# Kernel optimization log

Hardware: AMD Instinct MI355X
Metric: run time of the kernel (lower is better)

## Reference

```python
import jax, jax.numpy as jnp
import numpy as np

DIM = 2048
HEADS = 16
DIM_HEAD = 128
DIM_INNER = HEADS * DIM_HEAD
BATCH = 2
SEQ = 2048
EPS = 1e-12  # F.normalize default eps


def l2norm(t, axis=-1):
    # matches F.normalize(t, dim=axis, p=2): t / max(||t||, eps)
    n = jnp.sqrt(jnp.sum(t * t, axis=axis, keepdims=True))
    return t / jnp.maximum(n, EPS)


def setup_inputs() -> dict:
    key = jax.random.key(0)
    ks = jax.random.split(key, 5)
    x = jax.random.normal(ks[0], (BATCH, SEQ, DIM), dtype=jnp.float32)
    # NormLinear weights (torch Linear layout: [out, in]); parametrization
    # l2-normalizes rows (dim=-1) for q/k/v and columns (dim=0) for to_out.
    Wq = jax.random.normal(ks[1], (DIM_INNER, DIM), dtype=jnp.float32) / np.sqrt(DIM)
    Wk = jax.random.normal(ks[2], (DIM_INNER, DIM), dtype=jnp.float32) / np.sqrt(DIM)
    Wv = jax.random.normal(ks[3], (DIM_INNER, DIM), dtype=jnp.float32) / np.sqrt(DIM)
    Wout = jax.random.normal(ks[4], (DIM, DIM_INNER), dtype=jnp.float32) / np.sqrt(DIM_INNER)
    # Scale(dim_inner, init=1.0, scale=dim**-1): param = ones * dim**-1,
    # forward_scale = init/scale = dim, so qk_scale() starts at 1.0
    qk_scale = jnp.ones((DIM_INNER,), dtype=jnp.float32) / DIM
    return {"x": x, "Wq": Wq, "Wk": Wk, "Wv": Wv, "Wout": Wout, "qk_scale": qk_scale}


def reference(x, Wq, Wk, Wv, Wout, qk_scale):
    b, n, _ = x.shape
    # NormLinear: x @ l2norm(W, rows).T  (scale = groups**-1 = 1)
    q = jnp.einsum('bnd,ed->bne', x, l2norm(Wq, axis=-1))
    k = jnp.einsum('bnd,ed->bne', x, l2norm(Wk, axis=-1))
    v = jnp.einsum('bnd,ed->bne', x, l2norm(Wv, axis=-1))
    # split heads: b n (h d) -> b h n d
    split = lambda t: t.reshape(b, n, HEADS, DIM_HEAD).transpose(0, 2, 1, 3)
    q, k, v = split(q), split(k), split(v)
    # per-head l2norm of q and k over head dim
    q = l2norm(q, axis=-1)
    k = l2norm(k, axis=-1)
    # learned qk scale: (h d) -> h 1 d, effective = param * forward_scale(=DIM)
    q = q * (qk_scale * DIM).reshape(HEADS, 1, DIM_HEAD)
    # causal SDPA with scale = sqrt(dim_head) (unit-norm q,k in nGPT)
    attn_scale = DIM_HEAD ** 0.5
    scores = jnp.einsum('bhid,bhjd->bhij', q, k) * attn_scale
    causal = jnp.tril(jnp.ones((n, n), dtype=bool))
    scores = jnp.where(causal, scores, jnp.finfo(scores.dtype).min)
    attn = jax.nn.softmax(scores, axis=-1)
    out = jnp.einsum('bhij,bhjd->bhid', attn, v)
    # merge heads: b h n d -> b n (h d)
    out = out.transpose(0, 2, 1, 3).reshape(b, n, DIM_INNER)
    # to_out: NormLinear with norm over dim=0 of weight [DIM, DIM_INNER]
    out = jnp.einsum('bne,de->bnd', out, l2norm(Wout, axis=0))
    return out
```

## Files before the change

kernel.cpp:

```cpp
#include <hip/hip_runtime.h>


typedef __bf16 bf16x8 __attribute__((ext_vector_type(8)));
typedef float f32x4 __attribute__((ext_vector_type(4)));

__device__ __forceinline__ unsigned short f2bf(float f) {
  unsigned int u = __float_as_uint(f);
  u = u + 0x7FFFu + ((u >> 16) & 1u);
  return (unsigned short)(u >> 16);
}

__device__ __forceinline__ void async16(const void* g, void* l) {
  __builtin_amdgcn_global_load_lds(
      (const __attribute__((address_space(1))) unsigned int*)g,
      (__attribute__((address_space(3))) unsigned int*)l, 16, 0, 0);
}

#define QFOLD (2048.0f * 11.313708498984761f * 1.4426950408889634f)


__global__ __launch_bounds__(256) void prep_w_rows(
    const float* __restrict__ Wq, const float* __restrict__ Wk,
    const float* __restrict__ Wv, ushort* __restrict__ oq,
    ushort* __restrict__ ok_, ushort* __restrict__ ov) {
  const int row = blockIdx.x;
  const float* W = (blockIdx.y == 0) ? Wq : (blockIdx.y == 1) ? Wk : Wv;
  ushort* O = (blockIdx.y == 0) ? oq : (blockIdx.y == 1) ? ok_ : ov;
  const int t = threadIdx.x;
  const float4* Wr = (const float4*)(W + (size_t)row * 2048);
  float4 v0 = Wr[t];
  float4 v1 = Wr[t + 256];
  float ss = v0.x * v0.x + v0.y * v0.y + v0.z * v0.z + v0.w * v0.w +
             v1.x * v1.x + v1.y * v1.y + v1.z * v1.z + v1.w * v1.w;
  ss += __shfl_xor(ss, 1);  ss += __shfl_xor(ss, 2);
  ss += __shfl_xor(ss, 4);  ss += __shfl_xor(ss, 8);
  ss += __shfl_xor(ss, 16); ss += __shfl_xor(ss, 32);
  __shared__ float red[4];
  if ((t & 63) == 0) red[t >> 6] = ss;
  __syncthreads();
  float tot = red[0] + red[1] + red[2] + red[3];
  float sc = 1.0f / fmaxf(sqrtf(tot), 1e-12f);
  ushort4 o0, o1;
  o0.x = f2bf(v0.x * sc); o0.y = f2bf(v0.y * sc);
  o0.z = f2bf(v0.z * sc); o0.w = f2bf(v0.w * sc);
  o1.x = f2bf(v1.x * sc); o1.y = f2bf(v1.y * sc);
  o1.z = f2bf(v1.z * sc); o1.w = f2bf(v1.w * sc);
  *(ushort4*)(O + (size_t)row * 2048 + t * 4) = o0;
  *(ushort4*)(O + (size_t)row * 2048 + 1024 + t * 4) = o1;
}

__global__ __launch_bounds__(256) void wout_colss(const float* __restrict__ W,
                                                  float* __restrict__ colss) {
  const int e = blockIdx.x * 256 + threadIdx.x;
  const int d0 = blockIdx.y * 128;
  float ss = 0.f;
  #pragma unroll 8
  for (int i = 0; i < 128; ++i) {
    float v = W[(size_t)(d0 + i) * 2048 + e];
    ss += v * v;
  }
  atomicAdd(colss + e, ss);
}

__global__ __launch_bounds__(256) void wout_norm(const float* __restrict__ W,
                                                 const float* __restrict__ colss,
                                                 ushort* __restrict__ O) {
  const int idx = (blockIdx.x * 256 + threadIdx.x) * 4;
  float4 v = *(const float4*)(W + idx);
  float4 c = *(const float4*)(colss + (idx & 2047));
  ushort4 o;
  o.x = f2bf(v.x / fmaxf(sqrtf(c.x), 1e-12f));
  o.y = f2bf(v.y / fmaxf(sqrtf(c.y), 1e-12f));
  o.z = f2bf(v.z / fmaxf(sqrtf(c.z), 1e-12f));
  o.w = f2bf(v.w / fmaxf(sqrtf(c.w), 1e-12f));
  *(ushort4*)(O + idx) = o;
}

__global__ __launch_bounds__(256) void convert_x(const float* __restrict__ X,
                                                 ushort* __restrict__ O) {
  const int idx = (blockIdx.x * 256 + threadIdx.x) * 4;
  float4 v = *(const float4*)(X + idx);
  ushort4 o;
  o.x = f2bf(v.x); o.y = f2bf(v.y); o.z = f2bf(v.z); o.w = f2bf(v.w);
  *(ushort4*)(O + idx) = o;
}

__global__ __launch_bounds__(64) void qk_mhead(const float* __restrict__ qks,
                                               float* __restrict__ mh) {
  const int h = blockIdx.x, l = threadIdx.x;
  float m = fmaxf(fabsf(qks[h * 128 + l]), fabsf(qks[h * 128 + 64 + l]));
  m = fmaxf(m, __shfl_xor(m, 1));  m = fmaxf(m, __shfl_xor(m, 2));
  m = fmaxf(m, __shfl_xor(m, 4));  m = fmaxf(m, __shfl_xor(m, 8));
  m = fmaxf(m, __shfl_xor(m, 16)); m = fmaxf(m, __shfl_xor(m, 32));
  if (l == 0) mh[h] = m * QFOLD;
}

__device__ __forceinline__ void gemm_mainloop(
    const ushort* __restrict__ A, const ushort* __restrict__ Bw,
    int m0, int n0, ushort* As, ushort* Bs, f32x4 acc[4][4],
    int t, int l, int wm, int wn) {
  const int l15 = l & 15, l4 = l >> 4;
  const ushort* abase = A + (size_t)m0 * 2048;
  const ushort* bbase = Bw + (size_t)n0 * 2048;
  for (int kt = 0; kt < 32; ++kt) {
    const int k0 = kt * 64;
    __syncthreads();
    #pragma unroll
    for (int p = 0; p < 9; ++p) {
      int c = p * 256 + t;
      const ushort* src = abase;
      char* dst = (char*)As;
      int cc = c;
      if (c >= 1152) { cc = c - 1152; src = bbase; dst = (char*)Bs; }
      int r = cc / 9, dc = cc - r * 9;
      int dcc = (dc == 8) ? 0 : dc;
      async16(src + (size_t)r * 2048 + k0 + dcc * 8, dst + cc * 16);
    }
    __syncthreads();
    #pragma unroll
    for (int ks = 0; ks < 2; ++ks) {
      bf16x8 af[4], bg[4];
      #pragma unroll
      for (int f = 0; f < 4; ++f)
        af[f] = *(const bf16x8*)&As[(wm * 64 + f * 16 + l15) * 72 + ks * 32 + l4 * 8];
      #pragma unroll
      for (int f = 0; f < 4; ++f)
        bg[f] = *(const bf16x8*)&Bs[(wn * 64 + f * 16 + l15) * 72 + ks * 32 + l4 * 8];
      #pragma unroll
      for (int fm = 0; fm < 4; ++fm)
        #pragma unroll
        for (int fn = 0; fn < 4; ++fn)
          acc[fm][fn] = __builtin_amdgcn_mfma_f32_16x16x32_bf16(
              af[fm], bg[fn], acc[fm][fn], 0, 0, 0);
    }
  }
}

__global__ __launch_bounds__(256, 4) void gemm_qkv(
    const ushort* __restrict__ X, const ushort* __restrict__ Wq,
    const ushort* __restrict__ Wk, const ushort* __restrict__ Wv,
    const float* __restrict__ qks, ushort* __restrict__ qn,
    ushort* __restrict__ kn, ushort* __restrict__ vt) {
  const int z = blockIdx.z;
  const ushort* Bw = (z == 0) ? Wq : (z == 1) ? Wk : Wv;
  const int n0 = blockIdx.x * 128;
  const int m0 = blockIdx.y * 128;
  __shared__ __align__(16) ushort As[128 * 72];
  __shared__ __align__(16) ushort Bs[128 * 72];
  __shared__ float partials[2][128];
  const int t = threadIdx.x, w = t >> 6, l = t & 63;
  const int wm = w & 1, wn = w >> 1;
  const int l15 = l & 15, l4 = l >> 4;

  f32x4 acc[4][4];
  #pragma unroll
  for (int i = 0; i < 4; ++i)
    #pragma unroll
    for (int j = 0; j < 4; ++j) acc[i][j] = (f32x4){0.f, 0.f, 0.f, 0.f};

  gemm_mainloop(X, Bw, m0, n0, As, Bs, acc, t, l, wm, wn);

  const int h = n0 >> 7;
  if (z == 2) {
    #pragma unroll
    for (int fm = 0; fm < 4; ++fm) {
      int mrow = m0 + wm * 64 + fm * 16 + l4 * 4;
      int bb = mrow >> 11;
      int nn = mrow & 2047;
      #pragma unroll
      for (int fn = 0; fn < 4; ++fn) {
        int d = wn * 64 + fn * 16 + l15;
        ushort4 p;
        p.x = f2bf(acc[fm][fn][0]); p.y = f2bf(acc[fm][fn][1]);
        p.z = f2bf(acc[fm][fn][2]); p.w = f2bf(acc[fm][fn][3]);
        *(ushort4*)(vt + (size_t)((bb * 16 + h) * 128 + d) * 2048 + nn) = p;
      }
    }
  } else {
    float rs[4][4];
    #pragma unroll
    for (int fm = 0; fm < 4; ++fm)
      #pragma unroll
      for (int r = 0; r < 4; ++r) {
        float s = 0.f;
        #pragma unroll
        for (int fn = 0; fn < 4; ++fn) {
          float v = acc[fm][fn][r];
          s += v * v;
        }
        s += __shfl_xor(s, 1); s += __shfl_xor(s, 2);
        s += __shfl_xor(s, 4); s += __shfl_xor(s, 8);
        rs[fm][r] = s;
      }
    if (l15 == 0) {
      #pragma unroll
      for (int fm = 0; fm < 4; ++fm)
        #pragma unroll
        for (int r = 0; r < 4; ++r)
          partials[wn][wm * 64 + fm * 16 + l4 * 4 + r] = rs[fm][r];
    }
    __syncthreads();
    float cs[4];
    #pragma unroll
    for (int fn = 0; fn < 4; ++fn)
      cs[fn] = (z == 0) ? qks[n0 + wn * 64 + fn * 16 + l15] * QFOLD : 1.0f;
    ushort* O = (z == 0) ? qn : kn;
    #pragma unroll
    for (int fm = 0; fm < 4; ++fm)
      #pragma unroll
      for (int r = 0; r < 4; ++r) {
        int i = wm * 64 + fm * 16 + l4 * 4 + r;
        float tot = partials[0][i] + partials[1][i];
        float sc = 1.0f / fmaxf(sqrtf(tot), 1e-12f);
        #pragma unroll
        for (int fn = 0; fn < 4; ++fn)
          O[(size_t)(m0 + i) * 2048 + n0 + wn * 64 + fn * 16 + l15] =
              f2bf(acc[fm][fn][r] * sc * cs[fn]);
      }
  }
}

__global__ __launch_bounds__(256, 3) void attn_kernel(
    const ushort* __restrict__ qn, const ushort* __restrict__ kn,
    const ushort* __restrict__ vt, const float* __restrict__ mhead,
    ushort* __restrict__ ao) {
  const int hb = blockIdx.x;
  const int b = hb >> 4, h = hb & 15;
  const int qt = 31 - blockIdx.y;
  const int i0 = qt * 64;
  const int t = threadIdx.x, w = t >> 6, l = t & 63;
  const int l15 = l & 15, l4 = l >> 4;

  __shared__ __align__(16) ushort Ks[64 * 136];
  __shared__ __align__(16) ushort Vts[128 * 72];
  __shared__ __align__(16) ushort Ps[64 * 72];

  bf16x8 qf[4];
  #pragma unroll
  for (int ks = 0; ks < 4; ++ks)
    qf[ks] = *(const bf16x8*)(qn +
        (size_t)(b * 2048 + i0 + w * 16 + l15) * 2048 +
        h * 128 + ks * 32 + l4 * 8);

  f32x4 Oa[8];
  #pragma unroll
  for (int fd = 0; fd < 8; ++fd) Oa[fd] = (f32x4){0.f, 0.f, 0.f, 0.f};
  f32x4 Ol = (f32x4){0.f, 0.f, 0.f, 0.f};

  const float mh = mhead[h];
  const __bf16 one = (__bf16)1.0f;
  const bf16x8 ones = {one, one, one, one, one, one, one, one};

  const ushort* kbase = kn + (size_t)(b * 2048) * 2048 + h * 128;
  const ushort* vbase = vt + (size_t)((b * 16 + h) * 128) * 2048;

  for (int jt = 0; jt <= qt; ++jt) {
    const int j0 = jt * 64;
    __syncthreads();
    #pragma unroll
    for (int pass = 0; pass < 5; ++pass) {
      int c = pass * 256 + t;
      if (c < 1088) {
        int r = c / 17, dc = c - r * 17;
        int dcc = (dc == 16) ? 0 : dc;
        async16(kbase + (size_t)(j0 + r) * 2048 + dcc * 8, (char*)Ks + c * 16);
      }
    }
    #pragma unroll
    for (int pass = 0; pass < 5; ++pass) {
      int c = pass * 256 + t;
      if (c < 1152) {
        int r = c / 9, jc = c - r * 9;
        int jcc = (jc == 8) ? 0 : jc;
        async16(vbase + (size_t)r * 2048 + j0 + jcc * 8, (char*)Vts + c * 16);
      }
    }
    __syncthreads();

    f32x4 Sa[4];
    #pragma unroll
    for (int fj = 0; fj < 4; ++fj) {
      f32x4 s0 = (f32x4){0.f, 0.f, 0.f, 0.f};
      #pragma unroll
      for (int ks = 0; ks < 4; ++ks) {
        bf16x8 kf = *(const bf16x8*)&Ks[(fj * 16 + l15) * 136 + ks * 32 + l4 * 8];
        s0 = __builtin_amdgcn_mfma_f32_16x16x32_bf16(qf[ks], kf, s0, 0, 0, 0);
      }
      Sa[fj] = s0;
    }

    if (jt == qt) {
      #pragma unroll
      for (int fj = 0; fj < 4; ++fj)
        #pragma unroll
        for (int r = 0; r < 4; ++r) {
          int jg = fj * 16 + l15;
          int ig = w * 16 + l4 * 4 + r;
          if (jg > ig) Sa[fj][r] = -1e30f;
        }
    }

    #pragma unroll
    for (int fj = 0; fj < 4; ++fj)
      #pragma unroll
      for (int r = 0; r < 4; ++r)
        Ps[(w * 16 + l4 * 4 + r) * 72 + fj * 16 + l15] =
            f2bf(__builtin_exp2f(Sa[fj][r] - mh));

    #pragma unroll
    for (int ks = 0; ks < 2; ++ks) {
      bf16x8 p0 = *(const bf16x8*)&Ps[(w * 16 + l15) * 72 + ks * 32 + l4 * 8];
      Ol = __builtin_amdgcn_mfma_f32_16x16x32_bf16(p0, ones, Ol, 0, 0, 0);
      #pragma unroll
      for (int fd = 0; fd < 8; ++fd) {
        bf16x8 vf = *(const bf16x8*)&Vts[(fd * 16 + l15) * 72 + ks * 32 + l4 * 8];
        Oa[fd] = __builtin_amdgcn_mfma_f32_16x16x32_bf16(p0, vf, Oa[fd], 0, 0, 0);
      }
    }
  }

  #pragma unroll
  for (int r = 0; r < 4; ++r) {
    float inv = 1.0f / Ol[r];
    int ig = i0 + w * 16 + l4 * 4 + r;
    #pragma unroll
    for (int fd = 0; fd < 8; ++fd)
      ao[(size_t)(b * 2048 + ig) * 2048 + h * 128 + fd * 16 + l15] =
          f2bf(Oa[fd][r] * inv);
  }
}

__global__ __launch_bounds__(256, 4) void gemm_out(
    const ushort* __restrict__ A, const ushort* __restrict__ Bw,
    float* __restrict__ C) {
  const int n0 = blockIdx.x * 128;
  const int m0 = blockIdx.y * 128;
  __shared__ __align__(16) ushort As[128 * 72];
  __shared__ __align__(16) ushort Bs[128 * 72];
  const int t = threadIdx.x, w = t >> 6, l = t & 63;
  const int wm = w & 1, wn = w >> 1;
  const int l15 = l & 15, l4 = l >> 4;

  f32x4 acc[4][4];
  #pragma unroll
  for (int i = 0; i < 4; ++i)
    #pragma unroll
    for (int j = 0; j < 4; ++j) acc[i][j] = (f32x4){0.f, 0.f, 0.f, 0.f};

  gemm_mainloop(A, Bw, m0, n0, As, Bs, acc, t, l, wm, wn);

  #pragma unroll
  for (int fm = 0; fm < 4; ++fm)
    #pragma unroll
    for (int fn = 0; fn < 4; ++fn)
      #pragma unroll
      for (int r = 0; r < 4; ++r)
        C[(size_t)(m0 + wm * 64 + fm * 16 + l4 * 4 + r) * 2048 +
          n0 + wn * 64 + fn * 16 + l15] = acc[fm][fn][r];
}

extern "C" void kernel_launch(void* const* d_in, const int* in_sizes, int n_in,
                              void* d_out, int out_size, void* d_ws, size_t ws_size,
                              hipStream_t stream) {
  (void)in_sizes; (void)n_in; (void)out_size; (void)ws_size;
  const float* x    = (const float*)d_in[0];
  const float* Wq   = (const float*)d_in[1];
  const float* Wk   = (const float*)d_in[2];
  const float* Wv   = (const float*)d_in[3];
  const float* Wout = (const float*)d_in[4];
  const float* qks  = (const float*)d_in[5];
  char* ws = (char*)d_ws;

  ushort* wqn  = (ushort*)(ws + 0);
  ushort* wkn  = (ushort*)(ws + 8388608);
  ushort* wvn  = (ushort*)(ws + 16777216);
  ushort* wotn = (ushort*)(ws + 25165824);
  ushort* xbf  = (ushort*)(ws + 33554432);
  ushort* qn   = (ushort*)(ws + 50331648);
  ushort* kn   = (ushort*)(ws + 67108864);
  ushort* vt   = (ushort*)(ws + 83886080);
  ushort* ao   = (ushort*)(ws + 100663296);
  float* colss = (float*)(ws + 117440512);
  float* mh    = (float*)(ws + 117448704);
  float* out   = (float*)d_out;

  hipMemsetAsync(colss, 0, 2048 * sizeof(float), stream);
  prep_w_rows<<<dim3(2048, 3), 256, 0, stream>>>(Wq, Wk, Wv, wqn, wkn, wvn);
  wout_colss<<<dim3(8, 16), 256, 0, stream>>>(Wout, colss);
  wout_norm<<<4096, 256, 0, stream>>>(Wout, colss, wotn);
  convert_x<<<8192, 256, 0, stream>>>(x, xbf);
  qk_mhead<<<16, 64, 0, stream>>>(qks, mh);
  gemm_qkv<<<dim3(16, 32, 3), 256, 0, stream>>>(xbf, wqn, wkn, wvn, qks, qn, kn, vt);
  attn_kernel<<<dim3(32, 32), 256, 0, stream>>>(qn, kn, vt, mh, ao);
  gemm_out<<<dim3(16, 32), 256, 0, stream>>>(ao, wotn, out);
}
```

Measured before the change: 386.6 us.

## Use 256x128 triple-buffered GEMM mainloop with XOR-swizzled LDS and async prefetch

Replaces the single-buffered 128x128 GEMM mainloop, which synchronised twice per k-step, with a 256x128 tile over 8 waves. The new loop keeps three LDS stages and issues async global-to-LDS loads for future tiles in between the MFMA groups. LDS is XOR-swizzled instead of padded to avoid bank conflicts, and s_setprio is raised around the MFMA blocks. Both the QKV and output projections use the new loop. The cost is more LDS per block (about 144KB) and fewer resident blocks per CU, and correctness now depends on the hand-written vmcnt accounting.

```diff
diff --git a/kernel.cpp b/kernel.cpp
--- a/kernel.cpp
+++ b/kernel.cpp
@@ -95,78 +95,132 @@
   if (l == 0) mh[h] = m * QFOLD;
 }
 
-__device__ __forceinline__ void gemm_mainloop(
+
+#define LDSBUF 49152
+#define ABYTES 32768
+
+__device__ __forceinline__ void mainloop_256x128(
     const ushort* __restrict__ A, const ushort* __restrict__ Bw,
-    int m0, int n0, ushort* As, ushort* Bs, f32x4 acc[4][4],
-    int t, int l, int wm, int wn) {
+    int m0, int n0, char* lds, f32x4 acc[4][4], int t) {
+  const int l = t & 63, w = t >> 6;
+  const int wm = w & 3, wn = w >> 2;
   const int l15 = l & 15, l4 = l >> 4;
-  const ushort* abase = A + (size_t)m0 * 2048;
-  const ushort* bbase = Bw + (size_t)n0 * 2048;
-  for (int kt = 0; kt < 32; ++kt) {
-    const int k0 = kt * 64;
-    __syncthreads();
-    #pragma unroll
-    for (int p = 0; p < 9; ++p) {
-      int c = p * 256 + t;
-      const ushort* src = abase;
-      char* dst = (char*)As;
-      int cc = c;
-      if (c >= 1152) { cc = c - 1152; src = bbase; dst = (char*)Bs; }
-      int r = cc / 9, dc = cc - r * 9;
-      int dcc = (dc == 8) ? 0 : dc;
-      async16(src + (size_t)r * 2048 + k0 + dcc * 8, dst + cc * 16);
-    }
-    __syncthreads();
-    #pragma unroll
-    for (int ks = 0; ks < 2; ++ks) {
-      bf16x8 af[4], bg[4];
-      #pragma unroll
-      for (int f = 0; f < 4; ++f)
-        af[f] = *(const bf16x8*)&As[(wm * 64 + f * 16 + l15) * 72 + ks * 32 + l4 * 8];
-      #pragma unroll
-      for (int f = 0; f < 4; ++f)
-        bg[f] = *(const bf16x8*)&Bs[(wn * 64 + f * 16 + l15) * 72 + ks * 32 + l4 * 8];
+
+  const int lc = (t & 7) ^ ((t >> 3) & 7);
+  const ushort* srcA = A + (size_t)m0 * 2048 + (t >> 3) * 2048 + lc * 8;
+  const ushort* srcB = Bw + (size_t)n0 * 2048 + (t >> 3) * 2048 + lc * 8;
+  char* dstA = lds + t * 16;
+  char* dstB = lds + ABYTES + t * 16;
+
+  const int rdA = (wm * 64 + l15) * 128;
+  const int rdB = ABYTES + (wn * 64 + l15) * 128;
+  const int cb0 = ((l4 ^ (l15 & 7)) * 16);
+  const int cb1 = (((4 + l4) ^ (l15 & 7)) * 16);
+
+  auto stageA = [&](int s, int k0, int o) {
+    async16(srcA + (size_t)o * 131072 + k0, dstA + s * LDSBUF + o * 8192);
+  };
+  auto stageB = [&](int s, int k0, int o) {
+    async16(srcB + (size_t)o * 131072 + k0, dstB + s * LDSBUF + o * 8192);
+  };
+
+  #pragma unroll
+  for (int i = 0; i < 4; ++i)
+    #pragma unroll
+    for (int j = 0; j < 4; ++j) acc[i][j] = (f32x4){0.f, 0.f, 0.f, 0.f};
+
+  stageA(0, 0, 0); stageA(0, 0, 1); stageA(0, 0, 2); stageA(0, 0, 3);
+  stageB(0, 0, 0); stageB(0, 0, 1);
+  stageA(1, 64, 0); stageA(1, 64, 1); stageA(1, 64, 2); stageA(1, 64, 3);
+  stageB(1, 64, 0); stageB(1, 64, 1);
+  asm volatile("s_waitcnt vmcnt(6)" ::: "memory");
+  __builtin_amdgcn_s_barrier();
+
+  auto tile = [&](int s, int s2, int k2, bool pf) {
+    const char* Ab = lds + s * LDSBUF;
+    bf16x8 af[4][2], bg[4][2];
+    #pragma unroll
+    for (int fm = 0; fm < 4; ++fm) {
+      af[fm][0] = *(const bf16x8*)(Ab + rdA + fm * 2048 + cb0);
+      af[fm][1] = *(const bf16x8*)(Ab + rdA + fm * 2048 + cb1);
+    }
+    #pragma unroll
+    for (int fn = 0; fn < 2; ++fn) {
+      bg[fn][0] = *(const bf16x8*)(Ab + rdB + fn * 2048 + cb0);
+      bg[fn][1] = *(const bf16x8*)(Ab + rdB + fn * 2048 + cb1);
+    }
+    if (pf) { stageA(s2, k2, 0); stageA(s2, k2, 1); stageA(s2, k2, 2); }
+    __builtin_amdgcn_s_setprio(1);
+    #pragma unroll
+    for (int ks = 0; ks < 2; ++ks)
       #pragma unroll
       for (int fm = 0; fm < 4; ++fm)
         #pragma unroll
-        for (int fn = 0; fn < 4; ++fn)
+        for (int fn = 0; fn < 2; ++fn)
           acc[fm][fn] = __builtin_amdgcn_mfma_f32_16x16x32_bf16(
-              af[fm], bg[fn], acc[fm][fn], 0, 0, 0);
-    }
+              af[fm][ks], bg[fn][ks], acc[fm][fn], 0, 0, 0);
+    __builtin_amdgcn_s_setprio(0);
+    #pragma unroll
+    for (int fn = 2; fn < 4; ++fn) {
+      bg[fn][0] = *(const bf16x8*)(Ab + rdB + fn * 2048 + cb0);
+      bg[fn][1] = *(const bf16x8*)(Ab + rdB + fn * 2048 + cb1);
+    }
+    if (pf) { stageA(s2, k2, 3); stageB(s2, k2, 0); stageB(s2, k2, 1); }
+    __builtin_amdgcn_s_setprio(1);
+    #pragma unroll
+    for (int ks = 0; ks < 2; ++ks)
+      #pragma unroll
+      for (int fm = 0; fm < 4; ++fm)
+        #pragma unroll
+        for (int fn = 2; fn < 4; ++fn)
+          acc[fm][fn] = __builtin_amdgcn_mfma_f32_16x16x32_bf16(
+              af[fm][ks], bg[fn][ks], acc[fm][fn], 0, 0, 0);
+    __builtin_amdgcn_s_setprio(0);
+  };
+
+  #pragma unroll 1
+  for (int kt = 0; kt < 30; kt += 3) {
+    tile(0, 2, (kt + 2) * 64, true);
+    asm volatile("s_waitcnt vmcnt(6)" ::: "memory");
+    __builtin_amdgcn_s_barrier();
+    tile(1, 0, (kt + 3) * 64, true);
+    asm volatile("s_waitcnt vmcnt(6)" ::: "memory");
+    __builtin_amdgcn_s_barrier();
+    tile(2, 1, (kt + 4) * 64, true);
+    asm volatile("s_waitcnt vmcnt(6)" ::: "memory");
+    __builtin_amdgcn_s_barrier();
   }
-}
-
-__global__ __launch_bounds__(256, 4) void gemm_qkv(
+  tile(0, 0, 0, false);
+  asm volatile("s_waitcnt vmcnt(0)" ::: "memory");
+  __builtin_amdgcn_s_barrier();
+  tile(1, 0, 0, false);
+}
+
+__global__ __launch_bounds__(512, 2) void gemm_qkv(
     const ushort* __restrict__ X, const ushort* __restrict__ Wq,
     const ushort* __restrict__ Wk, const ushort* __restrict__ Wv,
     const float* __restrict__ qks, ushort* __restrict__ qn,
     ushort* __restrict__ kn, ushort* __restrict__ vt) {
+  __shared__ __align__(16) char lds[3 * LDSBUF];
+  __shared__ float partials[2][256];
   const int z = blockIdx.z;
   const ushort* Bw = (z == 0) ? Wq : (z == 1) ? Wk : Wv;
   const int n0 = blockIdx.x * 128;
-  const int m0 = blockIdx.y * 128;
-  __shared__ __align__(16) ushort As[128 * 72];
-  __shared__ __align__(16) ushort Bs[128 * 72];
-  __shared__ float partials[2][128];
-  const int t = threadIdx.x, w = t >> 6, l = t & 63;
-  const int wm = w & 1, wn = w >> 1;
+  const int m0 = blockIdx.y * 256;
+  const int t = threadIdx.x;
+  const int l = t & 63, w = t >> 6;
+  const int wm = w & 3, wn = w >> 2;
   const int l15 = l & 15, l4 = l >> 4;
 
   f32x4 acc[4][4];
-  #pragma unroll
-  for (int i = 0; i < 4; ++i)
-    #pragma unroll
-    for (int j = 0; j < 4; ++j) acc[i][j] = (f32x4){0.f, 0.f, 0.f, 0.f};
-
-  gemm_mainloop(X, Bw, m0, n0, As, Bs, acc, t, l, wm, wn);
-
-  const int h = n0 >> 7;
+  mainloop_256x128(X, Bw, m0, n0, lds, acc, t);
+
+  const int h = blockIdx.x;
   if (z == 2) {
+    const int bb = m0 >> 11, nb = m0 & 2047;
     #pragma unroll
     for (int fm = 0; fm < 4; ++fm) {
-      int mrow = m0 + wm * 64 + fm * 16 + l4 * 4;
-      int bb = mrow >> 11;
-      int nn = mrow & 2047;
+      int nn = nb + wm * 64 + fm * 16 + l4 * 4;
       #pragma unroll
       for (int fn = 0; fn < 4; ++fn) {
         int d = wn * 64 + fn * 16 + l15;
@@ -177,7 +231,6 @@
       }
     }
   } else {
-    float rs[4][4];
     #pragma unroll
     for (int fm = 0; fm < 4; ++fm)
       #pragma unroll
@@ -190,15 +243,8 @@
         }
         s += __shfl_xor(s, 1); s += __shfl_xor(s, 2);
         s += __shfl_xor(s, 4); s += __shfl_xor(s, 8);
-        rs[fm][r] = s;
-      }
-    if (l15 == 0) {
-      #pragma unroll
-      for (int fm = 0; fm < 4; ++fm)
-        #pragma unroll
-        for (int r = 0; r < 4; ++r)
-          partials[wn][wm * 64 + fm * 16 + l4 * 4 + r] = rs[fm][r];
-    }
+        if (l15 == 0) partials[wn][wm * 64 + fm * 16 + l4 * 4 + r] = s;
+      }
     __syncthreads();
     float cs[4];
     #pragma unroll
@@ -330,24 +376,19 @@
   }
 }
 
-__global__ __launch_bounds__(256, 4) void gemm_out(
+__global__ __launch_bounds__(512, 2) void gemm_out(
     const ushort* __restrict__ A, const ushort* __restrict__ Bw,
     float* __restrict__ C) {
+  __shared__ __align__(16) char lds[3 * LDSBUF];
   const int n0 = blockIdx.x * 128;
-  const int m0 = blockIdx.y * 128;
-  __shared__ __align__(16) ushort As[128 * 72];
-  __shared__ __align__(16) ushort Bs[128 * 72];
-  const int t = threadIdx.x, w = t >> 6, l = t & 63;
-  const int wm = w & 1, wn = w >> 1;
+  const int m0 = blockIdx.y * 256;
+  const int t = threadIdx.x;
+  const int l = t & 63, w = t >> 6;
+  const int wm = w & 3, wn = w >> 2;
   const int l15 = l & 15, l4 = l >> 4;
 
   f32x4 acc[4][4];
-  #pragma unroll
-  for (int i = 0; i < 4; ++i)
-    #pragma unroll
-    for (int j = 0; j < 4; ++j) acc[i][j] = (f32x4){0.f, 0.f, 0.f, 0.f};
-
-  gemm_mainloop(A, Bw, m0, n0, As, Bs, acc, t, l, wm, wn);
+  mainloop_256x128(A, Bw, m0, n0, lds, acc, t);
 
   #pragma unroll
   for (int fm = 0; fm < 4; ++fm)
@@ -390,7 +431,7 @@
   wout_norm<<<4096, 256, 0, stream>>>(Wout, colss, wotn);
   convert_x<<<8192, 256, 0, stream>>>(x, xbf);
   qk_mhead<<<16, 64, 0, stream>>>(qks, mh);
-  gemm_qkv<<<dim3(16, 32, 3), 256, 0, stream>>>(xbf, wqn, wkn, wvn, qks, qn, kn, vt);
+  gemm_qkv<<<dim3(16, 16, 3), 512, 0, stream>>>(xbf, wqn, wkn, wvn, qks, qn, kn, vt);
   attn_kernel<<<dim3(32, 32), 256, 0, stream>>>(qn, kn, vt, mh, ao);
-  gemm_out<<<dim3(16, 32), 256, 0, stream>>>(ao, wotn, out);
-}
+  gemm_out<<<dim3(16, 16), 512, 0, stream>>>(ao, wotn, out);
+}
```

Measured after the change: 376.5 us. -2.6%, faster.
